# Kernel tuning notes

Measured on AMD Instinct MI355X. Metric: run time of the kernel, lower is better.

Reference implementation:

```python
import jax, jax.numpy as jnp
import numpy as np

POOL_RATIO = 0.25
ROUTING_NUM = 3
B, N, D, H = 32, 2048, 512, 512


def setup_inputs() -> dict:
    key = jax.random.key(0)
    k_x, k_adj, k_w = jax.random.split(key, 3)
    x = jax.random.normal(k_x, (B, N, D), dtype=jnp.float32)
    # variable node counts per graph; row 0 uses all N nodes so max_cluster is static
    rng = np.random.default_rng(0)
    lens = np.full(B, N, dtype=np.int64)
    lens[1:] = rng.integers(N // 2, N + 1, size=B - 1)
    mask_np = (np.arange(N)[None, :] < lens[:, None])  # [B,N] bool
    mask = jnp.asarray(mask_np)
    # sparse-ish random adjacency, zeroed outside the node mask
    adj = (jax.random.uniform(k_adj, (B, N, N)) < 0.01).astype(jnp.float32)
    m = mask.astype(jnp.float32)
    adj = adj * m[:, None, :] * m[:, :, None]
    W = jax.random.normal(k_w, (D, H), dtype=jnp.float32) * 0.02
    b = jnp.zeros((H,), dtype=jnp.float32)
    return {"x": x, "adj": adj, "W": W, "b": b, "mask": mask}


def masked_softmax(s, m):
    # m: bool broadcastable to s; masked entries -> exactly 0 probability
    s = jnp.where(m, s, jnp.float32(-1e9))
    return jax.nn.softmax(s, axis=-1) * m


def squash(s):
    # squash along last (feature) dim, as in torch sum(dim=2) on [B,C,H]
    mag_sq = jnp.sum(s * s, axis=-1, keepdims=True)
    mag = jnp.sqrt(mag_sq)
    return mag_sq / (1.0 + mag_sq) * (s / mag)


def reference(x, adj, W, b, mask):
    fmask = mask.astype(x.dtype)
    node_num = fmask.sum(axis=1)                               # [B]
    cluster_num = jnp.floor(node_num * POOL_RATIO).astype(jnp.int32)
    max_cluster = int(x.shape[1] * POOL_RATIO)                 # static (row 0 has N nodes)
    cmask = jnp.arange(max_cluster)[None, :] < cluster_num[:, None]  # [B,C] bool
    cm = cmask[:, None, :]                                     # [B,1,C]
    # embed: dense GCN layer  z = relu(adj @ x @ W + b)  -> [B,N,H]
    z = jax.nn.relu(jnp.einsum('bnm,bmd,dh->bnh', adj, x, W) + b)
    s = jax.random.normal(jax.random.key(42), (x.shape[0], x.shape[1], max_cluster), dtype=x.dtype)
    for _ in range(ROUTING_NUM):
        s = masked_softmax(s, cm)                              # [B,N,C]
        xnext = squash(jnp.einsum('bnc,bnh->bch', s, z))       # [B,C,H]
        s = s + jnp.einsum('bnh,bch->bnc', z, xnext)           # routing update
    return masked_softmax(s, cm)
```

## Files before the change

### kernel.cpp

```cpp
#include <hip/hip_runtime.h>
#include <cstdint>
#include <cstddef>

#define NB 32
#define NN 2048
#define ND 512
#define NH 512
#define NC 512
#define ROWS (NB*NN)

typedef __attribute__((ext_vector_type(8))) short short8v;
typedef __attribute__((ext_vector_type(4))) float f32x4;

#define MFMA16(a,b,c) __builtin_amdgcn_mfma_f32_16x16x32_bf16((a),(b),(c),0,0,0)

typedef const __attribute__((address_space(1))) unsigned int* gas_t;
typedef __attribute__((address_space(3))) unsigned int* las_t;

__device__ __forceinline__ void gload16(const void* g, void* l){
  __builtin_amdgcn_global_load_lds((gas_t)g, (las_t)l, 16, 0, 0);
}

__device__ __forceinline__ void fsplit(float v, unsigned short& h, unsigned short& l){
  unsigned u = __float_as_uint(v);
  unsigned hb = (u + 0x7FFFu + ((u>>16)&1u)) >> 16;
  float hf = __uint_as_float(hb<<16);
  float r = v - hf;
  unsigned ur = __float_as_uint(r);
  l = (unsigned short)((ur + 0x7FFFu + ((ur>>16)&1u)) >> 16);
  h = (unsigned short)hb;
}

__device__ __forceinline__ unsigned rotl32(unsigned x, int d){ return (x<<d)|(x>>(32-d)); }

__device__ __forceinline__ unsigned threefry_xor(unsigned k0, unsigned k1, unsigned c0, unsigned c1){
  unsigned ks2 = 0x1BD11BDAu ^ k0 ^ k1;
  unsigned x0 = c0 + k0, x1 = c1 + k1;
#define TF_RND(r) { x0 += x1; x1 = rotl32(x1,(r)); x1 ^= x0; }
  TF_RND(13) TF_RND(15) TF_RND(26) TF_RND(6)
  x0 += k1;  x1 += ks2 + 1u;
  TF_RND(17) TF_RND(29) TF_RND(16) TF_RND(24)
  x0 += ks2; x1 += k0 + 2u;
  TF_RND(13) TF_RND(15) TF_RND(26) TF_RND(6)
  x0 += k0;  x1 += k1 + 3u;
  TF_RND(17) TF_RND(29) TF_RND(16) TF_RND(24)
  x0 += k1;  x1 += ks2 + 4u;
  TF_RND(13) TF_RND(15) TF_RND(26) TF_RND(6)
  x0 += ks2; x1 += k0 + 5u;
#undef TF_RND
  return x0 ^ x1;
}

__device__ __forceinline__ float bits_to_normal(unsigned bits){
  float f = __uint_as_float((bits >> 9) | 0x3f800000u) - 1.0f;
  const float lo = -0.99999994f;
  float u = fmaxf(lo, fmaf(f, 2.0f, lo));
  float w = -log1pf(-(u*u));
  float p;
  if (w < 5.0f){
    w -= 2.5f;
    p =            2.81022636e-08f;
    p = fmaf(p, w, 3.43273939e-07f);
    p = fmaf(p, w, -3.5233877e-06f);
    p = fmaf(p, w, -4.39150654e-06f);
    p = fmaf(p, w, 0.00021858087f);
    p = fmaf(p, w, -0.00125372503f);
    p = fmaf(p, w, -0.00417768164f);
    p = fmaf(p, w, 0.246640727f);
    p = fmaf(p, w, 1.50140941f);
  } else {
    w = sqrtf(w) - 3.0f;
    p =            -0.000200214257f;
    p = fmaf(p, w, 0.000100950558f);
    p = fmaf(p, w, 0.00134934322f);
    p = fmaf(p, w, -0.00367342844f);
    p = fmaf(p, w, 0.00573950773f);
    p = fmaf(p, w, -0.0076224613f);
    p = fmaf(p, w, 0.00943887047f);
    p = fmaf(p, w, 1.00167406f);
    p = fmaf(p, w, 2.83297682f);
  }
  return 1.4142135623730951f * (p * u);
}

__global__ void __launch_bounds__(256) rng_kernel(float* __restrict__ s){
  unsigned i = blockIdx.x * 256u + threadIdx.x;
  s[i] = bits_to_normal(threefry_xor(0u, 42u, 0u, i));
}

__global__ void __launch_bounds__(256) counts_kernel(const unsigned char* __restrict__ mraw,
                                                     int* __restrict__ cnum,
                                                     int* __restrict__ lenbuf){
  __shared__ int red[256];
  int b = blockIdx.x, tid = threadIdx.x;
  unsigned char b0 = mraw[0], b1 = mraw[1];
  int cnt = 0;
  if (b0 == 1 && b1 == 1){
    const unsigned char* p = mraw + (size_t)b * NN;
    for (int i = tid; i < NN; i += 256) cnt += (p[i] != 0);
  } else if (b0 == 1){
    const int* p = (const int*)mraw + (size_t)b * NN;
    for (int i = tid; i < NN; i += 256) cnt += (p[i] != 0);
  } else {
    const float* p = (const float*)mraw + (size_t)b * NN;
    for (int i = tid; i < NN; i += 256) cnt += (p[i] != 0.0f);
  }
  red[tid] = cnt; __syncthreads();
  for (int off = 128; off; off >>= 1){ if (tid < off) red[tid] += red[tid+off]; __syncthreads(); }
  if (tid == 0){ cnum[b] = red[0] >> 2; lenbuf[b] = red[0]; }
}

__global__ void __launch_bounds__(256) spmm_kernel(const float* __restrict__ adj,
                                                   const float* __restrict__ x,
                                                   unsigned short* __restrict__ yh,
                                                   unsigned short* __restrict__ yl,
                                                   const int* __restrict__ lenbuf){
  __shared__ int idxs[NN];
  __shared__ int wtot[4];
  int row = blockIdx.x;
  int b = row >> 11;
  int n = row & 2047;
  int tid = threadIdx.x;
  int l = tid & 63, w = tid >> 6;
  size_t base = (size_t)row * ND;
  if (n >= lenbuf[b]){
    yh[base+tid]=0; yl[base+tid]=0; yh[base+tid+256]=0; yl[base+tid+256]=0;
    return;
  }
  const float* arow = adj + (size_t)row * NN;
  float v[8];
  *(float4*)&v[0] = *(const float4*)(arow + tid*8);
  *(float4*)&v[4] = *(const float4*)(arow + tid*8 + 4);
  int lc = 0;
  #pragma unroll
  for (int j=0;j<8;j++) lc += (v[j] != 0.0f);
  int sc = lc;
  #pragma unroll
  for (int off=1; off<64; off<<=1){
    int t = __shfl_up(sc, off, 64);
    if (l >= off) sc += t;
  }
  if (l == 63) wtot[w] = sc;
  __syncthreads();
  int basep = 0;
  #pragma unroll
  for (int i=0;i<4;i++) if (i < w) basep += wtot[i];
  int total = wtot[0]+wtot[1]+wtot[2]+wtot[3];
  int pos = basep + sc - lc;
  #pragma unroll
  for (int j=0;j<8;j++){
    if (v[j] != 0.0f){ idxs[pos++] = tid*8 + j; }
  }
  __syncthreads();
  float acc0 = 0.f, acc1 = 0.f;
  const float* xb = x + (size_t)b * NN * ND;
  int j = 0;
  for (; j+4 <= total; j += 4){
    int m0_=idxs[j], m1_=idxs[j+1], m2_=idxs[j+2], m3_=idxs[j+3];
    float a0 = xb[(size_t)m0_*ND + tid], a1 = xb[(size_t)m1_*ND + tid];
    float a2 = xb[(size_t)m2_*ND + tid], a3 = xb[(size_t)m3_*ND + tid];
    float b0 = xb[(size_t)m0_*ND + tid + 256], b1 = xb[(size_t)m1_*ND + tid + 256];
    float b2 = xb[(size_t)m2_*ND + tid + 256], b3 = xb[(size_t)m3_*ND + tid + 256];
    acc0 += a0; acc0 += a1; acc0 += a2; acc0 += a3;
    acc1 += b0; acc1 += b1; acc1 += b2; acc1 += b3;
  }
  for (; j < total; j++){
    int m_ = idxs[j];
    acc0 += xb[(size_t)m_*ND + tid];
    acc1 += xb[(size_t)m_*ND + tid + 256];
  }
  unsigned short h,lo;
  fsplit(acc0,h,lo); yh[base+tid]=h;     yl[base+tid]=lo;
  fsplit(acc1,h,lo); yh[base+tid+256]=h; yl[base+tid+256]=lo;
}

__global__ void __launch_bounds__(256) wsplit_kernel(const float* __restrict__ W,
                                                     unsigned short* __restrict__ WTh,
                                                     unsigned short* __restrict__ WTl){
  __shared__ float t[32][33];
  int bx = blockIdx.x, by = blockIdx.y;
  int x = threadIdx.x & 31, y = threadIdx.x >> 5;
  for (int yy=y; yy<32; yy+=8) t[yy][x] = W[(size_t)(bx*32+yy)*512 + by*32 + x];
  __syncthreads();
  for (int yy=y; yy<32; yy+=8){
    float v = t[x][yy];
    unsigned short h,l; fsplit(v,h,l);
    size_t idx = (size_t)(by*32+yy)*512 + bx*32 + x;
    WTh[idx]=h; WTl[idx]=l;
  }
}

template<bool SPLIT, bool WF32>
__global__ void __launch_bounds__(256) softmax_kernel(float* __restrict__ s,
                                                      unsigned short* __restrict__ sh,
                                                      unsigned short* __restrict__ sl,
                                                      const int* __restrict__ cnum){
  int row  = blockIdx.x*4 + (threadIdx.x >> 6);
  int lane = threadIdx.x & 63;
  int b = row >> 11;
  int Kc = cnum[b];
  float* p = s + (size_t)row * NC;
  float4 v0 = *(const float4*)(p + lane*4);
  float4 v1 = *(const float4*)(p + lane*4 + 256);
  float e[8] = {v0.x,v0.y,v0.z,v0.w,v1.x,v1.y,v1.z,v1.w};
  float m = -3.0e38f;
  #pragma unroll
  for (int j=0;j<8;j++){
    int c = (j<4) ? lane*4 + j : lane*4 + 252 + j;
    if (c < Kc) m = fmaxf(m, e[j]);
  }
  #pragma unroll
  for (int off=32; off; off>>=1) m = fmaxf(m, __shfl_xor(m, off, 64));
  float r[8]; float sum = 0.f;
  #pragma unroll
  for (int j=0;j<8;j++){
    int c = (j<4) ? lane*4 + j : lane*4 + 252 + j;
    r[j] = (c < Kc) ? expf(e[j] - m) : 0.0f;
    sum += r[j];
  }
  #pragma unroll
  for (int off=32; off; off>>=1) sum += __shfl_xor(sum, off, 64);
  float inv = 1.0f / sum;
  #pragma unroll
  for (int j=0;j<8;j++) r[j] *= inv;
  if constexpr (WF32){
    *(float4*)(p + lane*4)       = make_float4(r[0],r[1],r[2],r[3]);
    *(float4*)(p + lane*4 + 256) = make_float4(r[4],r[5],r[6],r[7]);
  }
  if constexpr (SPLIT){
    unsigned long long ph=0, pl=0, qh=0, ql=0;
    #pragma unroll
    for (int j=0;j<4;j++){
      unsigned short h,l;
      fsplit(r[j],h,l);
      ph |= (unsigned long long)h << (16*j);  pl |= (unsigned long long)l << (16*j);
      fsplit(r[4+j],h,l);
      qh |= (unsigned long long)h << (16*j);  ql |= (unsigned long long)l << (16*j);
    }
    size_t base = (size_t)row * NC + lane*4;
    *(unsigned long long*)(sh + base)       = ph;
    *(unsigned long long*)(sl + base)       = pl;
    *(unsigned long long*)(sh + base + 256) = qh;
    *(unsigned long long*)(sl + base + 256) = ql;
  }
}

template<int EPI, bool SWZ>
__global__ void __launch_bounds__(256,2) gemm128_kernel(
    const unsigned short* __restrict__ Ah, const unsigned short* __restrict__ Al,
    const unsigned short* __restrict__ Bh, const unsigned short* __restrict__ Bl,
    unsigned short* __restrict__ OutH, unsigned short* __restrict__ OutL,
    float* __restrict__ Cf, const unsigned short* __restrict__ S2h,
    const unsigned short* __restrict__ S2l,
    const float* __restrict__ bias, const float* __restrict__ scale,
    const int* __restrict__ lenbuf, const int* __restrict__ cnumbuf,
    int K, long sA, long sB, long sC)
{
  __shared__ __align__(16) unsigned char smem[65536];
  int bx, by, bz;
  if constexpr (SWZ){
    int flat = blockIdx.x;
    int f2 = (flat & 7)*256 + (flat >> 3);
    bz = f2 >> 6; int rem = f2 & 63; bx = rem >> 2; by = rem & 3;
  } else { bx = blockIdx.x; by = blockIdx.y; bz = blockIdx.z; }
  Ah += (size_t)bz*sA; Al += (size_t)bz*sA;
  Bh += (size_t)bz*sB; Bl += (size_t)bz*sB;
  if constexpr (EPI==2){
    Cf += (size_t)bz*sC; S2h += (size_t)bz*sC; S2l += (size_t)bz*sC;
    scale += (size_t)bz*NC;
  }
  int m0 = bx*128, n0 = by*128;
  bool alive;
  if constexpr (EPI==1) alive = (m0 & 2047) < lenbuf[m0 >> 11];
  else                  alive = (m0 < lenbuf[bz]) && (n0 < cnumbuf[bz]);
  int tid = threadIdx.x;
  int l = tid & 63, wid = tid >> 6;
  int wr = wid >> 1, wc = wid & 1;
  int lr = l & 15, lk = l >> 4;

  f32x4 acc[4][4] = {};

  if (alive){
    int offA[4], offB[4];
    #pragma unroll
    for (int i=0;i<4;i++){
      int ra = wr*64 + i*16 + lr;
      offA[i] = ra*64 + ((lk ^ ((ra>>1)&3))<<4);
      int rb = wc*64 + i*16 + lr;
      offB[i] = rb*64 + ((lk ^ ((rb>>1)&3))<<4);
    }

    int srow = tid >> 2;
    int gslot = (tid & 3) ^ ((srow>>1)&3);
    const unsigned short* gA0 = Ah + (size_t)(m0 +      srow)*512 + gslot*8;
    const unsigned short* gA1 = Ah + (size_t)(m0 + 64 + srow)*512 + gslot*8;
    const unsigned short* gA2 = Al + (size_t)(m0 +      srow)*512 + gslot*8;
    const unsigned short* gA3 = Al + (size_t)(m0 + 64 + srow)*512 + gslot*8;
    const unsigned short* gB0 = Bh + (size_t)(n0 +      srow)*512 + gslot*8;
    const unsigned short* gB1 = Bh + (size_t)(n0 + 64 + srow)*512 + gslot*8;
    const unsigned short* gB2 = Bl + (size_t)(n0 +      srow)*512 + gslot*8;
    const unsigned short* gB3 = Bl + (size_t)(n0 + 64 + srow)*512 + gslot*8;

#define STAGE(buf, k0) { \
    unsigned char* db = smem + (buf)*32768 + wid*1024; \
    gload16(gA0 + (k0), db);          gload16(gA1 + (k0), db + 4096); \
    gload16(gA2 + (k0), db + 8192);   gload16(gA3 + (k0), db + 12288); \
    gload16(gB0 + (k0), db + 16384);  gload16(gB1 + (k0), db + 20480); \
    gload16(gB2 + (k0), db + 24576);  gload16(gB3 + (k0), db + 28672); }

    STAGE(0, 0)
    int KT = K >> 5;
    for (int t = 0; t < KT; ++t){
      asm volatile("s_waitcnt vmcnt(0)" ::: "memory");
      __syncthreads();
      if (t+1 < KT) STAGE((t+1)&1, (t+1)*32)
      const unsigned char* base = smem + (t&1)*32768;
      short8v ah[4], al[4], bh[4], bl[4];
      #pragma unroll
      for (int i=0;i<4;i++){
        ah[i] = *(const short8v*)(base + offA[i]);
        al[i] = *(const short8v*)(base + 8192 + offA[i]);
        bh[i] = *(const short8v*)(base + 16384 + offB[i]);
        bl[i] = *(const short8v*)(base + 24576 + offB[i]);
      }
      __builtin_amdgcn_s_setprio(1);
      #pragma unroll
      for (int i=0;i<4;i++)
        #pragma unroll
        for (int j=0;j<4;j++) acc[i][j] = MFMA16(ah[i], bh[j], acc[i][j]);
      #pragma unroll
      for (int i=0;i<4;i++)
        #pragma unroll
        for (int j=0;j<4;j++) acc[i][j] = MFMA16(ah[i], bl[j], acc[i][j]);
      #pragma unroll
      for (int i=0;i<4;i++)
        #pragma unroll
        for (int j=0;j<4;j++) acc[i][j] = MFMA16(al[i], bh[j], acc[i][j]);
      __builtin_amdgcn_s_setprio(0);
      __syncthreads();
    }
#undef STAGE
  }

  float aux[4];
  #pragma unroll
  for (int j=0;j<4;j++){
    int gcol = n0 + wc*64 + j*16 + lr;
    if constexpr (EPI==1) aux[j] = bias[gcol];
    if constexpr (EPI==2) aux[j] = scale[gcol];
  }
  #pragma unroll
  for (int i=0;i<4;i++){
    #pragma unroll
    for (int r=0;r<4;r++){
      int grow = m0 + wr*64 + i*16 + lk*4 + r;
      size_t rowb = (size_t)grow*512 + n0 + wc*64 + lr;
      #pragma unroll
      for (int j=0;j<4;j++){
        float v = acc[i][j][r];
        if constexpr (EPI==1){
          v = fmaxf(v + aux[j], 0.f);
          unsigned short h,lo2; fsplit(v,h,lo2);
          OutH[rowb + j*16] = h; OutL[rowb + j*16] = lo2;
        } else {
          unsigned hh = S2h[rowb + j*16], ll = S2l[rowb + j*16];
          float s2 = __uint_as_float(hh<<16) + __uint_as_float(ll<<16);
          Cf[rowb + j*16] = s2 + aux[j]*v;
        }
      }
    }
  }
}

__global__ void __launch_bounds__(256,2) gemmT128_kernel(
    const unsigned short* __restrict__ Ah, const unsigned short* __restrict__ Al,
    const unsigned short* __restrict__ Bh, const unsigned short* __restrict__ Bl,
    unsigned short* __restrict__ OutH, unsigned short* __restrict__ OutL,
    float* __restrict__ parts, const int* __restrict__ lenbuf,
    const int* __restrict__ cnumbuf)
{
  __shared__ __align__(16) unsigned char smem[65536];
  int flat = blockIdx.x;
  int f2 = (flat & 7)*64 + (flat >> 3);
  int bz = f2 >> 4; int rem = f2 & 15; int bx = rem >> 2; int by = rem & 3;
  size_t boff = (size_t)bz * NN * 512;
  Ah += boff; Al += boff; Bh += boff; Bl += boff;
  int m0 = bx*128, n0 = by*128;
  int KT = (lenbuf[bz] + 31) >> 5;
  int limc = cnumbuf[bz] - m0;
  bool alive = (limc > 0);
  int tid = threadIdx.x;
  int l = tid & 63, wid = tid >> 6;
  int wr = wid >> 1, wc = wid & 1;
  int lr = l & 15, lk = l >> 4;

  f32x4 acc[4][4] = {};

  if (alive){
    bool liA[4];
    int offA[4], offB[4];
    #pragma unroll
    for (int i=0;i<4;i++){
      int ra = wr*64 + i*16 + lr;
      offA[i] = ra*64 + ((lk ^ ((ra>>1)&3) ^ ((ra>>3)&3))<<4);
      liA[i] = (wr*64 + i*16) < limc;
      int rb = wc*64 + i*16 + lr;
      offB[i] = rb*64 + ((lk ^ ((rb>>1)&3) ^ ((rb>>3)&3))<<4);
    }

    int np  = tid & 15;
    int seg = tid >> 4;

    short8v ra0h, ra1h, ra0l, ra1l, rb0h, rb1h, rb0l, rb1l;

#define TLOAD(k0) { \
    size_t ga = (size_t)((k0) + 2*np)*512 + m0 + seg*8; \
    ra0h = *(const short8v*)(Ah + ga); ra1h = *(const short8v*)(Ah + ga + 512); \
    ra0l = *(const short8v*)(Al + ga); ra1l = *(const short8v*)(Al + ga + 512); \
    size_t gb = (size_t)((k0) + 2*np)*512 + n0 + seg*8; \
    rb0h = *(const short8v*)(Bh + gb); rb1h = *(const short8v*)(Bh + gb + 512); \
    rb0l = *(const short8v*)(Bl + gb); rb1l = *(const short8v*)(Bl + gb + 512); }

#define TWRITE(buf) { \
    unsigned char* bb = smem + (buf)*32768; \
    _Pragma("unroll") \
    for (int k=0;k<8;k++){ \
      int c = seg*8 + k; \
      int ps = (np>>2) ^ ((c>>1)&3) ^ ((c>>3)&3); \
      int byo = c*64 + ps*16 + (np&3)*4; \
      *(unsigned int*)(bb + byo)         = (unsigned int)(unsigned short)ra0h[k] | ((unsigned int)(unsigned short)ra1h[k]<<16); \
      *(unsigned int*)(bb + 8192 + byo)  = (unsigned int)(unsigned short)ra0l[k] | ((unsigned int)(unsigned short)ra1l[k]<<16); \
      *(unsigned int*)(bb + 16384 + byo) = (unsigned int)(unsigned short)rb0h[k] | ((unsigned int)(unsigned short)rb1h[k]<<16); \
      *(unsigned int*)(bb + 24576 + byo) = (unsigned int)(unsigned short)rb0l[k] | ((unsigned int)(unsigned short)rb1l[k]<<16); } }

    TLOAD(0)
    TWRITE(0)
    __syncthreads();
    for (int t = 0; t < KT; ++t){
      int more = (t+1 < KT);
      if (more) TLOAD((t+1)*32)
      const unsigned char* base = smem + (t&1)*32768;
      short8v ah[4], bh[4], bl[4];
      #pragma unroll
      for (int i=0;i<4;i++) if (liA[i]) ah[i] = *(const short8v*)(base + offA[i]);
      #pragma unroll
      for (int j=0;j<4;j++){
        bh[j] = *(const short8v*)(base + 16384 + offB[j]);
        bl[j] = *(const short8v*)(base + 24576 + offB[j]);
      }
      __builtin_amdgcn_s_setprio(1);
      #pragma unroll
      for (int i=0;i<4;i++) if (liA[i])
        #pragma unroll
        for (int j=0;j<4;j++) acc[i][j] = MFMA16(ah[i], bh[j], acc[i][j]);
      #pragma unroll
      for (int i=0;i<4;i++) if (liA[i])
        #pragma unroll
        for (int j=0;j<4;j++) acc[i][j] = MFMA16(ah[i], bl[j], acc[i][j]);
      #pragma unroll
      for (int i=0;i<4;i++) if (liA[i]){
        short8v al = *(const short8v*)(base + 8192 + offA[i]);
        #pragma unroll
        for (int j=0;j<4;j++) acc[i][j] = MFMA16(al, bh[j], acc[i][j]);
      }
      __builtin_amdgcn_s_setprio(0);
      if (more) TWRITE((t+1)&1)
      __syncthreads();
    }
#undef TLOAD
#undef TWRITE
  }

  #pragma unroll
  for (int i=0;i<4;i++){
    #pragma unroll
    for (int r=0;r<4;r++){
      int grow = m0 + wr*64 + i*16 + lk*4 + r;
      float p = 0.f;
      size_t rowb = (size_t)bz*NC*NH + (size_t)grow*512 + n0 + wc*64 + lr;
      #pragma unroll
      for (int j=0;j<4;j++){
        float v = acc[i][j][r];
        p = fmaf(v,v,p);
        unsigned short h,lo2; fsplit(v,h,lo2);
        OutH[rowb + j*16] = h; OutL[rowb + j*16] = lo2;
      }
      p += __shfl_xor(p, 1, 64);
      p += __shfl_xor(p, 2, 64);
      p += __shfl_xor(p, 4, 64);
      p += __shfl_xor(p, 8, 64);
      if (lr == 0) parts[(((size_t)bz*NC) + grow)*8 + by*2 + wc] = p;
    }
  }
}

__global__ void __launch_bounds__(512) scale_kernel(const float* __restrict__ parts,
                                                    float* __restrict__ scale){
  int b = blockIdx.x, c = threadIdx.x;
  const float* p = parts + ((size_t)b*NC + c)*8;
  float m2 = ((p[0]+p[1])+(p[2]+p[3])) + ((p[4]+p[5])+(p[6]+p[7]));
  float sc = 0.0f;
  if (m2 > 0.0f) sc = (m2/(1.0f+m2)) / sqrtf(m2);
  scale[(size_t)b*NC + c] = sc;
}

extern "C" void kernel_launch(void* const* d_in, const int* in_sizes, int n_in,
                              void* d_out, int out_size, void* d_ws, size_t ws_size,
                              hipStream_t stream) {
  const float* x    = (const float*)d_in[0];
  const float* adj  = (const float*)d_in[1];
  const float* W    = (const float*)d_in[2];
  const float* bias = (const float*)d_in[3];
  const unsigned char* mask = (const unsigned char*)d_in[4];
  float* out = (float*)d_out;
  char* ws = (char*)d_ws;

  unsigned short* zh   = (unsigned short*)(ws);
  unsigned short* zl   = (unsigned short*)(ws + 67108864);
  unsigned short* sth  = (unsigned short*)(ws + 134217728);
  unsigned short* stl  = (unsigned short*)(ws + 201326592);
  unsigned short* xnh  = (unsigned short*)(ws + 268435456);
  unsigned short* xnl  = (unsigned short*)(ws + 285212672);
  unsigned short* WTh  = (unsigned short*)(ws + 301989888);
  unsigned short* WTl  = (unsigned short*)(ws + 302514176);
  float* parts         = (float*)(ws + 303038464);
  float* scalebuf      = (float*)(ws + 304087040);
  int*   cnum          = (int*)(ws + 304152576);
  int*   lenbuf        = (int*)(ws + 304152704);
  unsigned short* yh = sth;
  unsigned short* yl = stl;

  counts_kernel<<<NB, 256, 0, stream>>>(mask, cnum, lenbuf);
  wsplit_kernel<<<dim3(16,16), 256, 0, stream>>>(W, WTh, WTl);
  spmm_kernel<<<ROWS, 256, 0, stream>>>(adj, x, yh, yl, lenbuf);
  gemm128_kernel<1,false><<<dim3(512,4,1), 256, 0, stream>>>(
      yh, yl, WTh, WTl, zh, zl, nullptr, nullptr, nullptr, bias, nullptr,
      lenbuf, cnum, ND, 0, 0, 0);
  rng_kernel<<<(ROWS*NC)/256, 256, 0, stream>>>(out);

  for (int it = 0; it < 3; ++it){
    softmax_kernel<true,false><<<ROWS/4, 256, 0, stream>>>(out, sth, stl, cnum);
    gemmT128_kernel<<<512, 256, 0, stream>>>(
        sth, stl, zh, zl, xnh, xnl, parts, lenbuf, cnum);
    scale_kernel<<<NB, 512, 0, stream>>>(parts, scalebuf);
    gemm128_kernel<2,true><<<2048, 256, 0, stream>>>(
        zh, zl, xnh, xnl, nullptr, nullptr, out, sth, stl, nullptr, scalebuf,
        lenbuf, cnum, NH, (long)NN*NH, (long)NC*NH, (long)NN*NC);
  }
  softmax_kernel<false,true><<<ROWS/4, 256, 0, stream>>>(out, nullptr, nullptr, cnum);
}
```

Measured before the change: 1.299 ms.

## Widen GEMM tile to 128x256 with single-buffered LDS and register prefetch

```diff
diff --git a/kernel.cpp b/kernel.cpp
--- a/kernel.cpp
+++ b/kernel.cpp
@@ -245,8 +245,8 @@
   }
 }
 
-template<int EPI, bool SWZ>
-__global__ void __launch_bounds__(256,2) gemm128_kernel(
+template<int EPI>
+__global__ void __launch_bounds__(256,2) gemmW_kernel(
     const unsigned short* __restrict__ Ah, const unsigned short* __restrict__ Al,
     const unsigned short* __restrict__ Bh, const unsigned short* __restrict__ Bl,
     unsigned short* __restrict__ OutH, unsigned short* __restrict__ OutL,
@@ -256,20 +256,19 @@
     const int* __restrict__ lenbuf, const int* __restrict__ cnumbuf,
     int K, long sA, long sB, long sC)
 {
-  __shared__ __align__(16) unsigned char smem[65536];
+  __shared__ __align__(16) unsigned char smem[49152];
+  int flat = blockIdx.x;
+  int f2 = (flat & 7)*128 + (flat >> 3);
   int bx, by, bz;
-  if constexpr (SWZ){
-    int flat = blockIdx.x;
-    int f2 = (flat & 7)*256 + (flat >> 3);
-    bz = f2 >> 6; int rem = f2 & 63; bx = rem >> 2; by = rem & 3;
-  } else { bx = blockIdx.x; by = blockIdx.y; bz = blockIdx.z; }
+  if constexpr (EPI==1){ bz = 0; bx = f2 >> 1; by = f2 & 1; }
+  else { bz = f2 >> 5; int rem = f2 & 31; bx = rem >> 1; by = rem & 1; }
   Ah += (size_t)bz*sA; Al += (size_t)bz*sA;
   Bh += (size_t)bz*sB; Bl += (size_t)bz*sB;
   if constexpr (EPI==2){
     Cf += (size_t)bz*sC; S2h += (size_t)bz*sC; S2l += (size_t)bz*sC;
     scale += (size_t)bz*NC;
   }
-  int m0 = bx*128, n0 = by*128;
+  int m0 = bx*128, n0 = by*256;
   bool alive;
   if constexpr (EPI==1) alive = (m0 & 2047) < lenbuf[m0 >> 11];
   else                  alive = (m0 < lenbuf[bz]) && (n0 < cnumbuf[bz]);
@@ -278,74 +277,78 @@
   int wr = wid >> 1, wc = wid & 1;
   int lr = l & 15, lk = l >> 4;
 
-  f32x4 acc[4][4] = {};
+  f32x4 acc[4][8] = {};
 
   if (alive){
-    int offA[4], offB[4];
+    int offA[4], offB[8];
     #pragma unroll
     for (int i=0;i<4;i++){
       int ra = wr*64 + i*16 + lr;
       offA[i] = ra*64 + ((lk ^ ((ra>>1)&3))<<4);
-      int rb = wc*64 + i*16 + lr;
-      offB[i] = rb*64 + ((lk ^ ((rb>>1)&3))<<4);
+    }
+    #pragma unroll
+    for (int j=0;j<8;j++){
+      int rb = wc*128 + j*16 + lr;
+      offB[j] = rb*64 + ((lk ^ ((rb>>1)&3))<<4);
     }
 
     int srow = tid >> 2;
     int gslot = (tid & 3) ^ ((srow>>1)&3);
-    const unsigned short* gA0 = Ah + (size_t)(m0 +      srow)*512 + gslot*8;
-    const unsigned short* gA1 = Ah + (size_t)(m0 + 64 + srow)*512 + gslot*8;
-    const unsigned short* gA2 = Al + (size_t)(m0 +      srow)*512 + gslot*8;
-    const unsigned short* gA3 = Al + (size_t)(m0 + 64 + srow)*512 + gslot*8;
-    const unsigned short* gB0 = Bh + (size_t)(n0 +      srow)*512 + gslot*8;
-    const unsigned short* gB1 = Bh + (size_t)(n0 + 64 + srow)*512 + gslot*8;
-    const unsigned short* gB2 = Bl + (size_t)(n0 +      srow)*512 + gslot*8;
-    const unsigned short* gB3 = Bl + (size_t)(n0 + 64 + srow)*512 + gslot*8;
-
-#define STAGE(buf, k0) { \
-    unsigned char* db = smem + (buf)*32768 + wid*1024; \
-    gload16(gA0 + (k0), db);          gload16(gA1 + (k0), db + 4096); \
-    gload16(gA2 + (k0), db + 8192);   gload16(gA3 + (k0), db + 12288); \
-    gload16(gB0 + (k0), db + 16384);  gload16(gB1 + (k0), db + 20480); \
-    gload16(gB2 + (k0), db + 24576);  gload16(gB3 + (k0), db + 28672); }
-
-    STAGE(0, 0)
+    const unsigned short* gAh = Ah + (size_t)(m0 + srow)*512 + gslot*8;
+    const unsigned short* gAl = Al + (size_t)(m0 + srow)*512 + gslot*8;
+    const unsigned short* gBh = Bh + (size_t)(n0 + srow)*512 + gslot*8;
+    const unsigned short* gBl = Bl + (size_t)(n0 + srow)*512 + gslot*8;
+    const size_t RS = (size_t)64*512;
+
+#define STAGEW(k0) { \
+    unsigned char* db = smem + wid*1024; \
+    gload16(gAh + (k0),        db);           gload16(gAh + (k0) + RS,   db + 4096); \
+    gload16(gAl + (k0),        db + 8192);    gload16(gAl + (k0) + RS,   db + 12288); \
+    gload16(gBh + (k0),        db + 16384);   gload16(gBh + (k0) + RS,   db + 20480); \
+    gload16(gBh + (k0) + 2*RS, db + 24576);   gload16(gBh + (k0) + 3*RS, db + 28672); \
+    gload16(gBl + (k0),        db + 32768);   gload16(gBl + (k0) + RS,   db + 36864); \
+    gload16(gBl + (k0) + 2*RS, db + 40960);   gload16(gBl + (k0) + 3*RS, db + 45056); }
+
+    STAGEW(0)
     int KT = K >> 5;
     for (int t = 0; t < KT; ++t){
       asm volatile("s_waitcnt vmcnt(0)" ::: "memory");
       __syncthreads();
-      if (t+1 < KT) STAGE((t+1)&1, (t+1)*32)
-      const unsigned char* base = smem + (t&1)*32768;
-      short8v ah[4], al[4], bh[4], bl[4];
+      short8v ah[4], al[4], bh[8], bl[8];
       #pragma unroll
       for (int i=0;i<4;i++){
-        ah[i] = *(const short8v*)(base + offA[i]);
-        al[i] = *(const short8v*)(base + 8192 + offA[i]);
-        bh[i] = *(const short8v*)(base + 16384 + offB[i]);
-        bl[i] = *(const short8v*)(base + 24576 + offB[i]);
+        ah[i] = *(const short8v*)(smem + offA[i]);
+        al[i] = *(const short8v*)(smem + 8192 + offA[i]);
       }
+      #pragma unroll
+      for (int j=0;j<8;j++){
+        bh[j] = *(const short8v*)(smem + 16384 + offB[j]);
+        bl[j] = *(const short8v*)(smem + 32768 + offB[j]);
+      }
+      __syncthreads();
+      if (t+1 < KT) STAGEW((t+1)*32)
       __builtin_amdgcn_s_setprio(1);
       #pragma unroll
       for (int i=0;i<4;i++)
         #pragma unroll
-        for (int j=0;j<4;j++) acc[i][j] = MFMA16(ah[i], bh[j], acc[i][j]);
+        for (int j=0;j<8;j++) acc[i][j] = MFMA16(ah[i], bh[j], acc[i][j]);
       #pragma unroll
       for (int i=0;i<4;i++)
         #pragma unroll
-        for (int j=0;j<4;j++) acc[i][j] = MFMA16(ah[i], bl[j], acc[i][j]);
+        for (int j=0;j<8;j++) acc[i][j] = MFMA16(ah[i], bl[j], acc[i][j]);
       #pragma unroll
       for (int i=0;i<4;i++)
         #pragma unroll
-        for (int j=0;j<4;j++) acc[i][j] = MFMA16(al[i], bh[j], acc[i][j]);
+        for (int j=0;j<8;j++) acc[i][j] = MFMA16(al[i], bh[j], acc[i][j]);
       __builtin_amdgcn_s_setprio(0);
-      __syncthreads();
-    }
-#undef STAGE
-  }
-
-  float aux[4];
-  #pragma unroll
-  for (int j=0;j<4;j++){
-    int gcol = n0 + wc*64 + j*16 + lr;
+    }
+#undef STAGEW
+  }
+
+  float aux[8];
+  #pragma unroll
+  for (int j=0;j<8;j++){
+    int gcol = n0 + wc*128 + j*16 + lr;
     if constexpr (EPI==1) aux[j] = bias[gcol];
     if constexpr (EPI==2) aux[j] = scale[gcol];
   }
@@ -354,9 +357,9 @@
     #pragma unroll
     for (int r=0;r<4;r++){
       int grow = m0 + wr*64 + i*16 + lk*4 + r;
-      size_t rowb = (size_t)grow*512 + n0 + wc*64 + lr;
-      #pragma unroll
-      for (int j=0;j<4;j++){
+      size_t rowb = (size_t)grow*512 + n0 + wc*128 + lr;
+      #pragma unroll
+      for (int j=0;j<8;j++){
         float v = acc[i][j][r];
         if constexpr (EPI==1){
           v = fmaxf(v + aux[j], 0.f);
@@ -533,7 +536,7 @@
   counts_kernel<<<NB, 256, 0, stream>>>(mask, cnum, lenbuf);
   wsplit_kernel<<<dim3(16,16), 256, 0, stream>>>(W, WTh, WTl);
   spmm_kernel<<<ROWS, 256, 0, stream>>>(adj, x, yh, yl, lenbuf);
-  gemm128_kernel<1,false><<<dim3(512,4,1), 256, 0, stream>>>(
+  gemmW_kernel<1><<<1024, 256, 0, stream>>>(
       yh, yl, WTh, WTl, zh, zl, nullptr, nullptr, nullptr, bias, nullptr,
       lenbuf, cnum, ND, 0, 0, 0);
   rng_kernel<<<(ROWS*NC)/256, 256, 0, stream>>>(out);
@@ -543,7 +546,7 @@
     gemmT128_kernel<<<512, 256, 0, stream>>>(
         sth, stl, zh, zl, xnh, xnl, parts, lenbuf, cnum);
     scale_kernel<<<NB, 512, 0, stream>>>(parts, scalebuf);
-    gemm128_kernel<2,true><<<2048, 256, 0, stream>>>(
+    gemmW_kernel<2><<<1024, 256, 0, stream>>>(
         zh, zl, xnh, xnl, nullptr, nullptr, out, sth, stl, nullptr, scalebuf,
         lenbuf, cnum, NH, (long)NN*NH, (long)NC*NH, (long)NN*NC);
   }
```

Result: no change. 1.297 ms (-0.2%).
